# Performance work log

Hardware: AMD Instinct MI355X
Metric: run time of the kernel (lower is better)

## Reference

```python
import jax, jax.numpy as jnp
import numpy as np

TOP_P = 0.9
NEG_FILL = -100000.0
POS_FILL = 100000.0


def setup_inputs() -> dict:
    key = jax.random.key(0)
    k1, k2, k3 = jax.random.split(key, 3)
    B, S, V = 256, 128, 128000
    input_ids = jax.random.randint(k1, (B, S), 0, V, dtype=jnp.int64)
    logits = jax.random.normal(k2, (B, V), dtype=jnp.float32)
    # uniform watermark keys xi in (0,1); avoid exact 0 for log
    xi = jax.random.uniform(k3, (V,), dtype=jnp.float32, minval=1e-6, maxval=1.0)
    return {"input_ids": input_ids, "logits": logits, "xi": xi}


def reference(input_ids, logits, xi):
    B, V = logits.shape
    probs = jax.nn.softmax(logits, axis=-1)                       # [B, V]
    order = jnp.argsort(-probs, axis=-1)                          # descending sort indices [B, V]
    sorted_probs = jnp.take_along_axis(probs, order, axis=-1)     # [B, V]
    cum = jnp.cumsum(sorted_probs, axis=-1)                       # [B, V]
    # torch.searchsorted(cum, top_p, right=False) == count of cum < top_p
    cutoff = jnp.sum(cum < TOP_P, axis=-1)                        # [B]
    keep = jnp.arange(V)[None, :] <= cutoff[:, None]              # keep [:cutoff+1]
    # exponential-minimum trick: argmin over -log(xi)/p within the top-p set
    scores = -jnp.log(xi[order]) / sorted_probs                   # [B, V]
    scores = jnp.where(keep, scores, jnp.inf)
    pos = jnp.argmin(scores, axis=-1)                             # [B]
    next_token = jnp.take_along_axis(order, pos[:, None], axis=-1)[:, 0]  # [B]
    out = jnp.full_like(logits, NEG_FILL)
    out = out.at[jnp.arange(B), next_token].set(POS_FILL)
    return out
```

## Files before the change

### kernel.cpp

```cpp
#include <hip/hip_runtime.h>
#include <hip/hip_bf16.h>
#include <math.h>


constexpr int   NBINS     = 4096;
constexpr int   CAP       = 1024;
constexpr float BIN_MIN   = -8.0f;
constexpr float BIN_SCALE = 256.0f;
constexpr float MASS_SCALE= 4096.0f;
constexpr float NEG_FILL  = -100000.0f;
constexpr float POS_FILL  =  100000.0f;
constexpr float TOPP      = 0.9f;
constexpr int   BPR_FILL  = 32;

struct Ws {
    float*  key;
    int*    binB;
    double* cumAbove;
    double* target;
    unsigned long long* winner;
};

__device__ __forceinline__ unsigned sortable(float f) {
    unsigned u = __float_as_uint(f);
    return (u & 0x80000000u) ? ~u : (u | 0x80000000u);
}
__device__ __forceinline__ int binOf(float l) {
    int b = (int)floorf((l - BIN_MIN) * BIN_SCALE);
    return min(max(b, 0), NBINS - 1);
}
__device__ __forceinline__ unsigned massOf(float l) {
    return __float2uint_rn(__expf(l) * MASS_SCALE);
}

__global__ __launch_bounds__(256)
void k0_key(const float4* __restrict__ xi4, float* __restrict__ key, int V4)
{
    const int stride = gridDim.x * 256;
    float4* key4 = reinterpret_cast<float4*>(key);
    for (int i = blockIdx.x * 256 + threadIdx.x; i < V4; i += stride) {
        float4 x = xi4[i];
        float4 k;
        k.x = __logf(-__logf(x.x));
        k.y = __logf(-__logf(x.y));
        k.z = __logf(-__logf(x.z));
        k.w = __logf(-__logf(x.w));
        key4[i] = k;
    }
}

__global__ __launch_bounds__(1024)
void kb_hist_scan(const float* __restrict__ logits, Ws ws, int V)
{
    const int row = blockIdx.x;
    const int tid = threadIdx.x;
    const int n4  = V >> 2;
    const float4* p4 = reinterpret_cast<const float4*>(logits + (size_t)row * V);

    __shared__ unsigned lh[NBINS];
    for (int i = tid; i < NBINS; i += 1024) lh[i] = 0u;
    __syncthreads();

    for (int base = 0; base < n4; base += 4096) {
        float4 r[4];
        int    j[4];
        #pragma unroll
        for (int u = 0; u < 4; ++u) {
            j[u] = base + u * 1024 + tid;
            if (j[u] < n4) r[u] = p4[j[u]];
        }
        #pragma unroll
        for (int u = 0; u < 4; ++u) {
            if (j[u] < n4) {
                float lv[4] = {r[u].x, r[u].y, r[u].z, r[u].w};
                #pragma unroll
                for (int c = 0; c < 4; ++c)
                    atomicAdd(&lh[binOf(lv[c])], massOf(lv[c]));
            }
        }
    }
    __syncthreads();

    if (tid < 64) {
        const int lane = tid;
        const int hi = NBINS - 1 - (lane << 6);
        double seg = 0.0;
        for (int k = 0; k < 64; ++k) seg += (double)lh[hi - k];

        double v = seg;
        for (int off = 1; off < 64; off <<= 1) {
            double u = __shfl_up(v, off);
            if (lane >= off) v += u;
        }
        double excl   = v - seg;
        double total  = __shfl(v, 63);
        double target = (double)TOPP * total;

        int    candBin = -1;
        double candS   = 0.0;
        double cum     = excl;
        for (int k = 0; k < 64; ++k) {
            int b = hi - k;
            double h = (double)lh[b];
            if (candBin < 0 && cum + h >= target) { candBin = b; candS = cum; }
            cum += h;
        }
        for (int off = 32; off >= 1; off >>= 1) {
            int    ob = __shfl_xor(candBin, off);
            double os = __shfl_xor(candS, off);
            if (ob > candBin) { candBin = ob; candS = os; }
        }
        if (lane == 0) {
            ws.binB[row]     = candBin;
            ws.cumAbove[row] = candS;
            ws.target[row]   = target;
        }
    }
}

__global__ __launch_bounds__(1024)
void kc_select(const float* __restrict__ logits, Ws ws, int V)
{
    const int row = blockIdx.x;
    const int tid = threadIdx.x;
    const int n4  = V >> 2;
    const float4* p4 = reinterpret_cast<const float4*>(logits + (size_t)row * V);
    const float4* k4 = reinterpret_cast<const float4*>(ws.key);
    const int binB = ws.binB[row];

    __shared__ float s_l[CAP];
    __shared__ float s_k[CAP];
    __shared__ unsigned s_m[CAP];
    __shared__ int   s_i[CAP];
    __shared__ int   s_cnt;
    __shared__ int   sKept;
    __shared__ unsigned long long wr[16];

    if (tid == 0) s_cnt = 0;
    __syncthreads();

    unsigned long long best = ~0ull;

    for (int base = 0; base < n4; base += 4096) {
        float4 r[4], x[4];
        int    j[4];
        #pragma unroll
        for (int u = 0; u < 4; ++u) {
            j[u] = base + u * 1024 + tid;
            if (j[u] < n4) { r[u] = p4[j[u]]; x[u] = k4[j[u]]; }
        }
        #pragma unroll
        for (int u = 0; u < 4; ++u) {
            if (j[u] < n4) {
                float lv[4] = {r[u].x, r[u].y, r[u].z, r[u].w};
                float kv[4] = {x[u].x, x[u].y, x[u].z, x[u].w};
                #pragma unroll
                for (int c = 0; c < 4; ++c) {
                    float l = lv[c];
                    int b = binOf(l);
                    if (b > binB) {
                        unsigned long long pack =
                            ((unsigned long long)sortable(kv[c] - l) << 32) |
                            (unsigned)(j[u] * 4 + c);
                        best = pack < best ? pack : best;
                    } else if (b == binB) {
                        int p = atomicAdd(&s_cnt, 1);
                        if (p < CAP) {
                            s_l[p] = l;
                            s_k[p] = kv[c] - l;
                            s_i[p] = j[u] * 4 + c;
                        }
                    }
                }
            }
        }
    }
    __syncthreads();

    int n = s_cnt; if (n > CAP) n = CAP;
    int P = 1; while (P < n) P <<= 1;
    if (P < 2) P = 2;
    for (int i = tid; i < P; i += 1024) {
        if (i >= n) { s_l[i] = -INFINITY; s_k[i] = 0.f; s_i[i] = 0x7fffffff; }
    }
    for (int size = 2; size <= P; size <<= 1) {
        for (int stride = size >> 1; stride > 0; stride >>= 1) {
            __syncthreads();
            if (tid < P) {
                int i = tid, jj = tid ^ stride;
                if (jj > i) {
                    float li = s_l[i], lj = s_l[jj];
                    int   ii = s_i[i], ij = s_i[jj];
                    bool up = ((i & size) == 0);
                    bool iBeforeJ = (li > lj) || (li == lj && ii < ij);
                    bool sw = up ? (!iBeforeJ && !(li == lj && ii == ij))
                                 : iBeforeJ;
                    if (sw) {
                        s_l[i] = lj; s_l[jj] = li;
                        float tk = s_k[i]; s_k[i] = s_k[jj]; s_k[jj] = tk;
                        s_i[i] = ij; s_i[jj] = ii;
                    }
                }
            }
        }
    }
    __syncthreads();

    for (int i = tid; i < n; i += 1024) s_m[i] = massOf(s_l[i]);
    __syncthreads();
    if (tid == 0) {
        double cum    = ws.cumAbove[row];
        double target = ws.target[row];
        int kept = n;
        for (int k = 0; k < n; ++k) {
            cum += (double)s_m[k];
            if (cum >= target) { kept = k + 1; break; }
        }
        sKept = kept;
    }
    __syncthreads();

    const int keptN = sKept;
    for (int k = tid; k < keptN; k += 1024) {
        unsigned long long pack =
            ((unsigned long long)sortable(s_k[k]) << 32) | (unsigned)s_i[k];
        best = pack < best ? pack : best;
    }
    for (int off = 32; off >= 1; off >>= 1) {
        unsigned long long o = __shfl_down(best, off);
        best = o < best ? o : best;
    }
    if ((tid & 63) == 0) wr[tid >> 6] = best;
    __syncthreads();
    if (tid == 0) {
        unsigned long long b = wr[0];
        for (int w = 1; w < 16; ++w) b = wr[w] < b ? wr[w] : b;
        ws.winner[row] = b;
    }
}

__global__ __launch_bounds__(256)
void kd_fill(float* __restrict__ out,
             const unsigned long long* __restrict__ winner, int V)
{
    const int row = blockIdx.x / BPR_FILL;
    const int seg = blockIdx.x % BPR_FILL;
    const int n4  = V >> 2;
    const int per = n4 / BPR_FILL;
    float4* o4 = reinterpret_cast<float4*>(out + (size_t)row * V) + seg * per;

    const unsigned win = (unsigned)(winner[row] & 0xffffffffu);
    const int local = (int)(win >> 2) - seg * per;

    const float4 nf = make_float4(NEG_FILL, NEG_FILL, NEG_FILL, NEG_FILL);
    for (int j = threadIdx.x; j < per; j += 256) {
        float4 v = nf;
        if (j == local) {
            float ov[4] = {v.x, v.y, v.z, v.w};
            ov[win & 3] = POS_FILL;
            v = make_float4(ov[0], ov[1], ov[2], ov[3]);
        }
        o4[j] = v;
    }
}

extern "C" void kernel_launch(void* const* d_in, const int* in_sizes, int n_in,
                              void* d_out, int out_size, void* d_ws, size_t ws_size,
                              hipStream_t stream) {
    const float* logits = (const float*)d_in[1];
    const float* xi     = (const float*)d_in[2];
    float*       out    = (float*)d_out;
    const int V = in_sizes[2];
    const int B = in_sizes[1] / V;

    char* w = (char*)d_ws;
    size_t off = 0;
    Ws ws;
    ws.key      = (float*)(w + off);  off += (size_t)V * sizeof(float);
    off = (off + 255) & ~(size_t)255;
    ws.binB     = (int*)(w + off);    off += (size_t)B * sizeof(int);
    off = (off + 255) & ~(size_t)255;
    ws.cumAbove = (double*)(w + off); off += (size_t)B * sizeof(double);
    ws.target   = (double*)(w + off); off += (size_t)B * sizeof(double);
    ws.winner   = (unsigned long long*)(w + off); off += (size_t)B * sizeof(unsigned long long);

    k0_key      <<<128, 256, 0, stream>>>((const float4*)xi, ws.key, V / 4);
    kb_hist_scan<<<B, 1024, 0, stream>>>(logits, ws, V);
    kc_select   <<<B, 1024, 0, stream>>>(logits, ws, V);
    kd_fill     <<<B * BPR_FILL, 256, 0, stream>>>(out, ws.winner, V);
}
```

Before: 300.1 us.

## Fuse histogram and selection into one row kernel with sampled pre-pass and candidate keys

Merges the histogram/scan and select kernels into one per-row kernel. A sampled histogram predicts the cutoff bin, and during the full pass elements near that bin are stashed in shared memory, so the second read of logits is avoided. The winner search only checks a small precomputed set of low-key vocabulary candidates (key < -3), with a full-row fallback when a bound check fails. The histogram now stores counts weighted by bin-centre exp instead of per-element mass, and kd_fill is fixed to cover the row tail. The trade-offs are more shared-memory use and an approximate mass per bin, which the exact in-bin sort and fallback are meant to correct.

```diff
diff --git a/kernel.cpp b/kernel.cpp
--- a/kernel.cpp
+++ b/kernel.cpp
@@ -4,20 +4,25 @@
 
 
 constexpr int   NBINS     = 4096;
-constexpr int   CAP       = 1024;
 constexpr float BIN_MIN   = -8.0f;
 constexpr float BIN_SCALE = 256.0f;
-constexpr float MASS_SCALE= 4096.0f;
+constexpr float BIN_OFF   = 2048.0f;
+constexpr float BIN_W     = 1.0f / 256.0f;
+constexpr int   STASH_CAP = 4096;
+constexpr int   BINB_CAP  = 512;
+constexpr int   WIN       = 6;
+constexpr int   MAXC      = 96;
+constexpr float CAND_THR  = -3.0f;
 constexpr float NEG_FILL  = -100000.0f;
 constexpr float POS_FILL  =  100000.0f;
 constexpr float TOPP      = 0.9f;
 constexpr int   BPR_FILL  = 32;
 
 struct Ws {
-    float*  key;
-    int*    binB;
-    double* cumAbove;
-    double* target;
+    float*    key;
+    unsigned* candIdx;
+    float*    candKey;
+    int*      candCnt;
     unsigned long long* winner;
 };
 
@@ -26,179 +31,213 @@
     return (u & 0x80000000u) ? ~u : (u | 0x80000000u);
 }
 __device__ __forceinline__ int binOf(float l) {
-    int b = (int)floorf((l - BIN_MIN) * BIN_SCALE);
+    int b = (int)fmaf(l, BIN_SCALE, BIN_OFF);
     return min(max(b, 0), NBINS - 1);
 }
-__device__ __forceinline__ unsigned massOf(float l) {
-    return __float2uint_rn(__expf(l) * MASS_SCALE);
-}
 
 __global__ __launch_bounds__(256)
-void k0_key(const float4* __restrict__ xi4, float* __restrict__ key, int V4)
+void k0_keys(const float4* __restrict__ xi4, float* __restrict__ key,
+             unsigned* __restrict__ candIdx, float* __restrict__ candKey,
+             int* __restrict__ candCnt, int V4)
 {
-    const int stride = gridDim.x * 256;
-    float4* key4 = reinterpret_cast<float4*>(key);
-    for (int i = blockIdx.x * 256 + threadIdx.x; i < V4; i += stride) {
-        float4 x = xi4[i];
-        float4 k;
-        k.x = __logf(-__logf(x.x));
-        k.y = __logf(-__logf(x.y));
-        k.z = __logf(-__logf(x.z));
-        k.w = __logf(-__logf(x.w));
-        key4[i] = k;
+    __shared__ int cnt;
+    __shared__ unsigned sIdx[MAXC];
+    __shared__ float    sKey[MAXC];
+    if (threadIdx.x == 0) cnt = 0;
+    __syncthreads();
+
+    const int f = blockIdx.x * 256 + threadIdx.x;
+    if (f < V4) {
+        float4 x = xi4[f];
+        float kv[4];
+        kv[0] = __logf(-__logf(x.x));
+        kv[1] = __logf(-__logf(x.y));
+        kv[2] = __logf(-__logf(x.z));
+        kv[3] = __logf(-__logf(x.w));
+        reinterpret_cast<float4*>(key)[f] = make_float4(kv[0], kv[1], kv[2], kv[3]);
+        #pragma unroll
+        for (int c = 0; c < 4; ++c) {
+            if (kv[c] < CAND_THR) {
+                int p = atomicAdd(&cnt, 1);
+                if (p < MAXC) { sIdx[p] = (unsigned)(f * 4 + c); sKey[p] = kv[c]; }
+            }
+        }
+    }
+    __syncthreads();
+    const int base = blockIdx.x * MAXC;
+    const int n = min(cnt, MAXC);
+    for (int i = threadIdx.x; i < MAXC; i += 256) {
+        candIdx[base + i] = (i < n) ? sIdx[i] : 0u;
+        candKey[base + i] = (i < n) ? sKey[i] : INFINITY;
+    }
+    if (threadIdx.x == 0) candCnt[blockIdx.x] = cnt;
+}
+
+__device__ __forceinline__ void scan_bins(const unsigned* lh, int lane,
+                                          int& candBin, double& candS, double& target)
+{
+    const int hi = NBINS - 1 - (lane << 6);
+    double seg = 0.0;
+    for (int k = 0; k < 64; ++k) {
+        int b = hi - k;
+        seg += (double)lh[b] * (double)__expf(fmaf((float)b + 0.5f, BIN_W, BIN_MIN));
+    }
+    double v = seg;
+    for (int off = 1; off < 64; off <<= 1) {
+        double u = __shfl_up(v, off);
+        if (lane >= off) v += u;
+    }
+    double excl = v - seg;
+    double total = __shfl(v, 63);
+    target = TOPP * total;
+
+    candBin = -1; candS = 0.0;
+    double cum = excl;
+    for (int k = 0; k < 64; ++k) {
+        int b = hi - k;
+        double h = (double)lh[b] * (double)__expf(fmaf((float)b + 0.5f, BIN_W, BIN_MIN));
+        if (candBin < 0 && cum + h >= target) { candBin = b; candS = cum; }
+        cum += h;
+    }
+    for (int off = 32; off >= 1; off >>= 1) {
+        int    ob = __shfl_xor(candBin, off);
+        double os = __shfl_xor(candS, off);
+        if (ob > candBin) { candBin = ob; candS = os; }
     }
 }
 
 __global__ __launch_bounds__(1024)
-void kb_hist_scan(const float* __restrict__ logits, Ws ws, int V)
+void kb_row(const float* __restrict__ logits, const float* __restrict__ key,
+            const unsigned* __restrict__ candIdx, const float* __restrict__ candKey,
+            const int* __restrict__ candCnt, unsigned long long* __restrict__ winner,
+            int V, int nchunk, int nslots)
 {
     const int row = blockIdx.x;
     const int tid = threadIdx.x;
     const int n4  = V >> 2;
-    const float4* p4 = reinterpret_cast<const float4*>(logits + (size_t)row * V);
+    const float* rowp = logits + (size_t)row * V;
+    const float4* p4 = reinterpret_cast<const float4*>(rowp);
 
     __shared__ unsigned lh[NBINS];
+    __shared__ float  s_sl[STASH_CAP];
+    __shared__ int    s_si[STASH_CAP];
+    __shared__ float  s_bl[BINB_CAP];
+    __shared__ int    s_bi[BINB_CAP];
+    __shared__ double s_be[BINB_CAP];
+    __shared__ unsigned long long wrd[16];
+    __shared__ float  wrf[16];
+    __shared__ int   sStashCnt, sB2, sBtil, sB, sM, sNeedFull, sCandOver;
+    __shared__ float sLmax, sLcut;
+    __shared__ int   sIcut;
+    __shared__ double sCumAbove, sTarget;
+    __shared__ unsigned long long sBest;
+
     for (int i = tid; i < NBINS; i += 1024) lh[i] = 0u;
-    __syncthreads();
-
-    for (int base = 0; base < n4; base += 4096) {
-        float4 r[4];
-        int    j[4];
+    if (tid == 0) { sStashCnt = 0; sB2 = 0; sCandOver = 0; sNeedFull = 0; }
+    __syncthreads();
+    if (tid < nchunk && candCnt[tid] > MAXC) atomicOr(&sCandOver, 1);
+
+    for (int k = 0; k < 8; ++k) {
+        int j = tid + k * 4000;
+        float4 L = p4[j];
+        atomicAdd(&lh[binOf(L.x)], 1u);
+        atomicAdd(&lh[binOf(L.y)], 1u);
+        atomicAdd(&lh[binOf(L.z)], 1u);
+        atomicAdd(&lh[binOf(L.w)], 1u);
+    }
+    __syncthreads();
+    if (tid < 64) {
+        int b; double cs, tg;
+        scan_bins(lh, tid, b, cs, tg);
+        if (tid == 0) sBtil = b;
+    }
+    __syncthreads();
+    const int wlo = max(0, sBtil - WIN);
+    const int whi = min(NBINS - 1, sBtil + WIN);
+
+    for (int i = tid; i < NBINS; i += 1024) lh[i] = 0u;
+    __syncthreads();
+
+    float lmax = -INFINITY;
+    for (int j = tid; j < n4; j += 1024) {
+        float4 L = p4[j];
+        float lv[4] = {L.x, L.y, L.z, L.w};
         #pragma unroll
-        for (int u = 0; u < 4; ++u) {
-            j[u] = base + u * 1024 + tid;
-            if (j[u] < n4) r[u] = p4[j[u]];
-        }
-        #pragma unroll
-        for (int u = 0; u < 4; ++u) {
-            if (j[u] < n4) {
-                float lv[4] = {r[u].x, r[u].y, r[u].z, r[u].w};
-                #pragma unroll
-                for (int c = 0; c < 4; ++c)
-                    atomicAdd(&lh[binOf(lv[c])], massOf(lv[c]));
-            }
-        }
+        for (int c = 0; c < 4; ++c) {
+            float l = lv[c];
+            int b = binOf(l);
+            atomicAdd(&lh[b], 1u);
+            lmax = fmaxf(lmax, l);
+            if ((unsigned)(b - wlo) <= (unsigned)(whi - wlo)) {
+                int p = atomicAdd(&sStashCnt, 1);
+                if (p < STASH_CAP) { s_sl[p] = l; s_si[p] = j * 4 + c; }
+            }
+        }
+    }
+    for (int off = 32; off >= 1; off >>= 1)
+        lmax = fmaxf(lmax, __shfl_down(lmax, off));
+    if ((tid & 63) == 0) wrf[tid >> 6] = lmax;
+    __syncthreads();
+    if (tid == 0) {
+        float m = wrf[0];
+        for (int w = 1; w < 16; ++w) m = fmaxf(m, wrf[w]);
+        sLmax = m;
     }
     __syncthreads();
 
     if (tid < 64) {
-        const int lane = tid;
-        const int hi = NBINS - 1 - (lane << 6);
-        double seg = 0.0;
-        for (int k = 0; k < 64; ++k) seg += (double)lh[hi - k];
-
-        double v = seg;
-        for (int off = 1; off < 64; off <<= 1) {
-            double u = __shfl_up(v, off);
-            if (lane >= off) v += u;
-        }
-        double excl   = v - seg;
-        double total  = __shfl(v, 63);
-        double target = (double)TOPP * total;
-
-        int    candBin = -1;
-        double candS   = 0.0;
-        double cum     = excl;
-        for (int k = 0; k < 64; ++k) {
-            int b = hi - k;
-            double h = (double)lh[b];
-            if (candBin < 0 && cum + h >= target) { candBin = b; candS = cum; }
-            cum += h;
-        }
-        for (int off = 32; off >= 1; off >>= 1) {
-            int    ob = __shfl_xor(candBin, off);
-            double os = __shfl_xor(candS, off);
-            if (ob > candBin) { candBin = ob; candS = os; }
-        }
-        if (lane == 0) {
-            ws.binB[row]     = candBin;
-            ws.cumAbove[row] = candS;
-            ws.target[row]   = target;
-        }
-    }
-}
-
-__global__ __launch_bounds__(1024)
-void kc_select(const float* __restrict__ logits, Ws ws, int V)
-{
-    const int row = blockIdx.x;
-    const int tid = threadIdx.x;
-    const int n4  = V >> 2;
-    const float4* p4 = reinterpret_cast<const float4*>(logits + (size_t)row * V);
-    const float4* k4 = reinterpret_cast<const float4*>(ws.key);
-    const int binB = ws.binB[row];
-
-    __shared__ float s_l[CAP];
-    __shared__ float s_k[CAP];
-    __shared__ unsigned s_m[CAP];
-    __shared__ int   s_i[CAP];
-    __shared__ int   s_cnt;
-    __shared__ int   sKept;
-    __shared__ unsigned long long wr[16];
-
-    if (tid == 0) s_cnt = 0;
-    __syncthreads();
-
-    unsigned long long best = ~0ull;
-
-    for (int base = 0; base < n4; base += 4096) {
-        float4 r[4], x[4];
-        int    j[4];
-        #pragma unroll
-        for (int u = 0; u < 4; ++u) {
-            j[u] = base + u * 1024 + tid;
-            if (j[u] < n4) { r[u] = p4[j[u]]; x[u] = k4[j[u]]; }
-        }
-        #pragma unroll
-        for (int u = 0; u < 4; ++u) {
-            if (j[u] < n4) {
-                float lv[4] = {r[u].x, r[u].y, r[u].z, r[u].w};
-                float kv[4] = {x[u].x, x[u].y, x[u].z, x[u].w};
-                #pragma unroll
-                for (int c = 0; c < 4; ++c) {
-                    float l = lv[c];
-                    int b = binOf(l);
-                    if (b > binB) {
-                        unsigned long long pack =
-                            ((unsigned long long)sortable(kv[c] - l) << 32) |
-                            (unsigned)(j[u] * 4 + c);
-                        best = pack < best ? pack : best;
-                    } else if (b == binB) {
-                        int p = atomicAdd(&s_cnt, 1);
-                        if (p < CAP) {
-                            s_l[p] = l;
-                            s_k[p] = kv[c] - l;
-                            s_i[p] = j[u] * 4 + c;
-                        }
-                    }
+        int b; double cs, tg;
+        scan_bins(lh, tid, b, cs, tg);
+        if (tid == 0) { sB = b; sCumAbove = cs; sTarget = tg; }
+    }
+    __syncthreads();
+    const int B = sB;
+
+    const bool stashOK = (B >= wlo) && (B <= whi) && (sStashCnt <= STASH_CAP);
+    if (stashOK) {
+        const int n = sStashCnt;
+        for (int i = tid; i < n; i += 1024) {
+            float l = s_sl[i];
+            if (binOf(l) == B) {
+                int q = atomicAdd(&sB2, 1);
+                if (q < BINB_CAP) { s_bl[q] = l; s_bi[q] = s_si[i]; }
+            }
+        }
+    } else {
+        for (int j = tid; j < n4; j += 1024) {
+            float4 L = p4[j];
+            float lv[4] = {L.x, L.y, L.z, L.w};
+            #pragma unroll
+            for (int c = 0; c < 4; ++c) {
+                if (binOf(lv[c]) == B) {
+                    int q = atomicAdd(&sB2, 1);
+                    if (q < BINB_CAP) { s_bl[q] = lv[c]; s_bi[q] = j * 4 + c; }
                 }
             }
         }
     }
     __syncthreads();
-
-    int n = s_cnt; if (n > CAP) n = CAP;
-    int P = 1; while (P < n) P <<= 1;
+    int nB = min(sB2, BINB_CAP);
+    if (sB2 > BINB_CAP && tid == 0) sNeedFull = 1;
+
+    int P = 1; while (P < nB) P <<= 1;
     if (P < 2) P = 2;
-    for (int i = tid; i < P; i += 1024) {
-        if (i >= n) { s_l[i] = -INFINITY; s_k[i] = 0.f; s_i[i] = 0x7fffffff; }
-    }
+    for (int i = tid; i < P; i += 1024)
+        if (i >= nB) { s_bl[i] = -INFINITY; s_bi[i] = 0x7fffffff; }
     for (int size = 2; size <= P; size <<= 1) {
         for (int stride = size >> 1; stride > 0; stride >>= 1) {
             __syncthreads();
             if (tid < P) {
                 int i = tid, jj = tid ^ stride;
                 if (jj > i) {
-                    float li = s_l[i], lj = s_l[jj];
-                    int   ii = s_i[i], ij = s_i[jj];
+                    float li = s_bl[i], lj = s_bl[jj];
+                    int   ii = s_bi[i], ij = s_bi[jj];
                     bool up = ((i & size) == 0);
                     bool iBeforeJ = (li > lj) || (li == lj && ii < ij);
-                    bool sw = up ? (!iBeforeJ && !(li == lj && ii == ij))
-                                 : iBeforeJ;
+                    bool sw = up ? (!iBeforeJ && !(li == lj && ii == ij)) : iBeforeJ;
                     if (sw) {
-                        s_l[i] = lj; s_l[jj] = li;
-                        float tk = s_k[i]; s_k[i] = s_k[jj]; s_k[jj] = tk;
-                        s_i[i] = ij; s_i[jj] = ii;
+                        s_bl[i] = lj; s_bl[jj] = li;
+                        s_bi[i] = ij; s_bi[jj] = ii;
                     }
                 }
             }
@@ -206,37 +245,76 @@
     }
     __syncthreads();
 
-    for (int i = tid; i < n; i += 1024) s_m[i] = massOf(s_l[i]);
+    for (int i = tid; i < nB; i += 1024) s_be[i] = exp((double)s_bl[i]);
     __syncthreads();
     if (tid == 0) {
-        double cum    = ws.cumAbove[row];
-        double target = ws.target[row];
-        int kept = n;
-        for (int k = 0; k < n; ++k) {
-            cum += (double)s_m[k];
-            if (cum >= target) { kept = k + 1; break; }
-        }
-        sKept = kept;
-    }
-    __syncthreads();
-
-    const int keptN = sKept;
-    for (int k = tid; k < keptN; k += 1024) {
-        unsigned long long pack =
-            ((unsigned long long)sortable(s_k[k]) << 32) | (unsigned)s_i[k];
-        best = pack < best ? pack : best;
+        double cum = sCumAbove, target = sTarget;
+        int m = nB;
+        for (int k = 0; k < nB; ++k) {
+            cum += s_be[k];
+            if (cum >= target) { m = k + 1; break; }
+        }
+        m = max(m, 1);
+        sM = m;
+        sLcut = s_bl[m - 1];
+        sIcut = s_bi[m - 1];
+    }
+    __syncthreads();
+    const float lcut = sLcut;
+    const int   icut = sIcut;
+
+    unsigned long long best = ~0ull;
+    for (int s = tid; s < nslots; s += 1024) {
+        unsigned idx = candIdx[s];
+        float ck = candKey[s];
+        float l = rowp[idx];
+        bool kept = (l > lcut) || (l == lcut && (int)idx <= icut);
+        if (kept) {
+            unsigned long long pack =
+                ((unsigned long long)sortable(ck - l) << 32) | idx;
+            best = pack < best ? pack : best;
+        }
     }
     for (int off = 32; off >= 1; off >>= 1) {
         unsigned long long o = __shfl_down(best, off);
         best = o < best ? o : best;
     }
-    if ((tid & 63) == 0) wr[tid >> 6] = best;
+    if ((tid & 63) == 0) wrd[tid >> 6] = best;
     __syncthreads();
     if (tid == 0) {
-        unsigned long long b = wr[0];
-        for (int w = 1; w < 16; ++w) b = wr[w] < b ? wr[w] : b;
-        ws.winner[row] = b;
-    }
+        unsigned long long b = wrd[0];
+        for (int w = 1; w < 16; ++w) b = wrd[w] < b ? wrd[w] : b;
+        sBest = b;
+        unsigned bound = sortable(CAND_THR - sLmax);
+        if (!((unsigned)(b >> 32) < bound) || sCandOver) sNeedFull = 1;
+    }
+    __syncthreads();
+
+    if (sNeedFull) {
+        for (int j = tid; j < V; j += 1024) {
+            float l = rowp[j];
+            bool kept = (l > lcut) || (l == lcut && j <= icut);
+            if (kept) {
+                unsigned long long pack =
+                    ((unsigned long long)sortable(key[j] - l) << 32) | (unsigned)j;
+                best = pack < best ? pack : best;
+            }
+        }
+        for (int off = 32; off >= 1; off >>= 1) {
+            unsigned long long o = __shfl_down(best, off);
+            best = o < best ? o : best;
+        }
+        if ((tid & 63) == 0) wrd[tid >> 6] = best;
+        __syncthreads();
+        if (tid == 0) {
+            unsigned long long b = sBest;
+            for (int w = 0; w < 16; ++w) b = wrd[w] < b ? wrd[w] : b;
+            sBest = b;
+        }
+        __syncthreads();
+    }
+
+    if (tid == 0) winner[row] = sBest;
 }
 
 __global__ __launch_bounds__(256)
@@ -247,15 +325,17 @@
     const int seg = blockIdx.x % BPR_FILL;
     const int n4  = V >> 2;
     const int per = n4 / BPR_FILL;
-    float4* o4 = reinterpret_cast<float4*>(out + (size_t)row * V) + seg * per;
+    const int start = seg * per;
+    const int end = (seg == BPR_FILL - 1) ? n4 : start + per;
+    float4* o4 = reinterpret_cast<float4*>(out + (size_t)row * V);
 
     const unsigned win = (unsigned)(winner[row] & 0xffffffffu);
-    const int local = (int)(win >> 2) - seg * per;
+    const int winj = (int)(win >> 2);
 
     const float4 nf = make_float4(NEG_FILL, NEG_FILL, NEG_FILL, NEG_FILL);
-    for (int j = threadIdx.x; j < per; j += 256) {
+    for (int j = start + threadIdx.x; j < end; j += 256) {
         float4 v = nf;
-        if (j == local) {
+        if (j == winj) {
             float ov[4] = {v.x, v.y, v.z, v.w};
             ov[win & 3] = POS_FILL;
             v = make_float4(ov[0], ov[1], ov[2], ov[3]);
@@ -272,20 +352,24 @@
     float*       out    = (float*)d_out;
     const int V = in_sizes[2];
     const int B = in_sizes[1] / V;
+    const int V4 = V / 4;
+    const int nchunk = (V + 1023) / 1024;
+    const int nslots = nchunk * MAXC;
 
     char* w = (char*)d_ws;
     size_t off = 0;
     Ws ws;
-    ws.key      = (float*)(w + off);  off += (size_t)V * sizeof(float);
+    ws.key     = (float*)(w + off);    off += (size_t)V * sizeof(float);
     off = (off + 255) & ~(size_t)255;
-    ws.binB     = (int*)(w + off);    off += (size_t)B * sizeof(int);
+    ws.candIdx = (unsigned*)(w + off); off += (size_t)nslots * sizeof(unsigned);
+    ws.candKey = (float*)(w + off);    off += (size_t)nslots * sizeof(float);
+    ws.candCnt = (int*)(w + off);      off += (size_t)nchunk * sizeof(int);
     off = (off + 255) & ~(size_t)255;
-    ws.cumAbove = (double*)(w + off); off += (size_t)B * sizeof(double);
-    ws.target   = (double*)(w + off); off += (size_t)B * sizeof(double);
-    ws.winner   = (unsigned long long*)(w + off); off += (size_t)B * sizeof(unsigned long long);
-
-    k0_key      <<<128, 256, 0, stream>>>((const float4*)xi, ws.key, V / 4);
-    kb_hist_scan<<<B, 1024, 0, stream>>>(logits, ws, V);
-    kc_select   <<<B, 1024, 0, stream>>>(logits, ws, V);
-    kd_fill     <<<B * BPR_FILL, 256, 0, stream>>>(out, ws.winner, V);
-}
+    ws.winner  = (unsigned long long*)(w + off); off += (size_t)B * sizeof(unsigned long long);
+
+    k0_keys<<<(V4 + 255) / 256, 256, 0, stream>>>((const float4*)xi, ws.key,
+                                                  ws.candIdx, ws.candKey, ws.candCnt, V4);
+    kb_row <<<B, 1024, 0, stream>>>(logits, ws.key, ws.candIdx, ws.candKey,
+                                    ws.candCnt, ws.winner, V, nchunk, nslots);
+    kd_fill<<<B * BPR_FILL, 256, 0, stream>>>(out, ws.winner, V);
+}
```

Measured after the change: 291.2 us. 1.03x faster.
